# Kernel tuning notes

Measured on AMD Instinct MI355X. Metric: run time of the kernel, lower is better.

## Reference

```python
import jax, jax.numpy as jnp
import numpy as np

SEQ, BATCH, HID = 4096, 32, 512


def setup_inputs() -> dict:
    key = jax.random.key(0)
    ks = jax.random.split(key, 7)
    s = 1.0 / np.sqrt(HID)
    return {
        "x0": jax.random.normal(ks[0], (SEQ, BATCH, 1), dtype=jnp.float32),
        "W_ih": jax.random.uniform(ks[1], (4 * HID, 1), jnp.float32, -s, s),
        "W_hh": jax.random.uniform(ks[2], (4 * HID, HID), jnp.float32, -s, s),
        "b_ih": jax.random.uniform(ks[3], (4 * HID,), jnp.float32, -s, s),
        "b_hh": jax.random.uniform(ks[4], (4 * HID,), jnp.float32, -s, s),
        "W_lin": jax.random.uniform(ks[5], (1, HID), jnp.float32, -s, s),
        "b_lin": jax.random.uniform(ks[6], (1,), jnp.float32, -s, s),
    }


def _lstm(x0, W_ih, W_hh, b_ih, b_hh):
    # x0: (T, B, 1). Precompute input contribution to gates for all steps.
    x_proj = jnp.einsum("tbi,gi->tbg", x0, W_ih) + (b_ih + b_hh)  # (T, B, 4H)
    T, B, _ = x_proj.shape
    H = W_hh.shape[1]
    h0 = jnp.zeros((B, H), x0.dtype)
    c0 = jnp.zeros((B, H), x0.dtype)

    def step(carry, xp):
        h, c = carry
        gates = xp + h @ W_hh.T  # (B, 4H)
        i, f, g, o = jnp.split(gates, 4, axis=-1)  # torch gate order i,f,g,o
        i = jax.nn.sigmoid(i)
        f = jax.nn.sigmoid(f)
        g = jnp.tanh(g)
        o = jax.nn.sigmoid(o)
        c = f * c + i * g
        h = o * jnp.tanh(c)
        return (h, c), h

    _, hs = jax.lax.scan(step, (h0, c0), x_proj)  # hs: (T, B, H)
    return hs


def reference(x0, W_ih, W_hh, b_ih, b_hh, W_lin, b_lin):
    hs = _lstm(x0, W_ih, W_hh, b_ih, b_hh)            # (T, B, H)
    y = jnp.einsum("tbh,oh->tbo", hs, W_lin) + b_lin  # (T, B, 1)
    return y + x0                                      # residual add
```

## Files before the change

### kernel.cpp

```cpp
#include <hip/hip_runtime.h>
#include <stdint.h>

#define T_STEPS 4096
#define BATCH 32
#define HID 512
#define GROUPS 8
#define BLK_THREADS 1024
#define NBLOCKS 256
#define SLOT_DW (BATCH * GROUPS * 64)

typedef _Float16 h2_t __attribute__((ext_vector_type(2)));
typedef uint32_t u32x8 __attribute__((ext_vector_type(8)));

__device__ inline uint32_t pack_h2(float a, float b) {
  h2_t v;
  v.x = (_Float16)a;
  v.y = (_Float16)b;
  return __builtin_bit_cast(uint32_t, v);
}

__device__ inline float fdot2(uint32_t a, uint32_t b, float c) {
  return __builtin_amdgcn_fdot2(__builtin_bit_cast(h2_t, a),
                                __builtin_bit_cast(h2_t, b), c, false);
}

__device__ inline uint64_t uni64(const void* p) {
  uint32_t lo = __builtin_amdgcn_readfirstlane((uint32_t)(uintptr_t)p);
  uint32_t hi = __builtin_amdgcn_readfirstlane((uint32_t)((uintptr_t)p >> 32));
  return ((uint64_t)hi << 32) | lo;
}

__device__ inline void kinv() {
  asm volatile("s_dcache_inv" ::: "memory");
}

__device__ inline void sload_rec(uint64_t p, u32x8* d0, u32x8* d1,
                                 u32x8* d2, u32x8* d3,
                                 uint32_t* t0, uint32_t* t1,
                                 uint32_t* t2, uint32_t* t3) {
  asm volatile("s_load_dwordx8 %0, %8, 0x0\n\t"
               "s_load_dword %4, %8, 0x20\n\t"
               "s_load_dwordx8 %1, %8, 0x40\n\t"
               "s_load_dword %5, %8, 0x60\n\t"
               "s_load_dwordx8 %2, %8, 0x80\n\t"
               "s_load_dword %6, %8, 0xa0\n\t"
               "s_load_dwordx8 %3, %8, 0xc0\n\t"
               "s_load_dword %7, %8, 0xe0\n\t"
               "s_waitcnt lgkmcnt(0)"
               : "=&s"(*d0), "=&s"(*d1), "=&s"(*d2), "=&s"(*d3),
                 "=&s"(*t0), "=&s"(*t1), "=&s"(*t2), "=&s"(*t3)
               : "s"(p) : "memory");
}

__device__ inline float sigf(float x) { return 1.0f / (1.0f + __expf(-x)); }
__device__ inline float tanh_fast(float x) {
  float a = fabsf(x);
  float e = __expf(-2.0f * a);
  float r = (1.0f - e) / (1.0f + e);
  return copysignf(r, x);
}

__global__ __launch_bounds__(BLK_THREADS)
void lstm_nobar(const float* __restrict__ x0,
                const float* __restrict__ W_ih,
                const float* __restrict__ W_hh,
                const float* __restrict__ b_ih,
                const float* __restrict__ b_hh,
                const float* __restrict__ W_lin,
                const float* __restrict__ b_lin,
                float* __restrict__ y,
                uint32_t* __restrict__ h_ex,
                int* __restrict__ claim)
{
  __shared__ float x0_lds[T_STEPS];
  __shared__ float ylds[T_STEPS];
  __shared__ float gacc[2][256];
  __shared__ int arrive[2];
  __shared__ int s_bg;

  const int tid = threadIdx.x;

  if (tid == 0) {
    uint32_t xcc;
    asm volatile("s_getreg_b32 %0, hwreg(HW_REG_XCC_ID)" : "=s"(xcc));
    xcc &= 7;
    int slot = atomicAdd(claim + xcc * 16, 1);
    s_bg = (slot < 32) ? (int)(((4 * xcc + (slot >> 3)) << 3) | (slot & 7))
                       : -1;
  }
  __syncthreads();
  if (s_bg < 0) return;
  const int b  = s_bg >> 3;
  const int g  = s_bg & 7;
  const int u0 = g * 64;
  const int wv = tid >> 6;
  const int rg = wv >> 3;
  const int cs = wv & 7;
  const int l  = tid & 63;

  uint32_t w0[32], w1[32];
  {
    const int r0 = 128 * rg + l;
    const int r1 = r0 + 64;
    const int R0 = (r0 >> 6) * HID + u0 + (r0 & 63);
    const int R1 = (r1 >> 6) * HID + u0 + (r1 & 63);
    const float2* p0 = (const float2*)(W_hh + (size_t)R0 * HID + 64 * cs);
    const float2* p1 = (const float2*)(W_hh + (size_t)R1 * HID + 64 * cs);
#pragma unroll
    for (int k = 0; k < 32; ++k) {
      float2 a = p0[k], c = p1[k];
      w0[k] = pack_h2(a.x, a.y);
      w1[k] = pack_h2(c.x, c.y);
    }
  }
  for (int i = tid; i < T_STEPS; i += BLK_THREADS) {
    x0_lds[i] = x0[i * BATCH + b];
    ylds[i] = 0.f;
  }
  if (tid < 256) { gacc[0][tid] = 0.f; gacc[1][tid] = 0.f; }
  if (tid < 2) arrive[tid] = 0;

  float c_state = 0.f;
  float wih_[4] = {0.f, 0.f, 0.f, 0.f}, bs_[4] = {0.f, 0.f, 0.f, 0.f};
  float wlin_u = 0.f, blin = 0.f;
  if (tid < 64) {
#pragma unroll
    for (int j = 0; j < 4; ++j) {
      int R = j * HID + u0 + tid;
      wih_[j] = W_ih[R];
      bs_[j] = b_ih[R] + b_hh[R];
    }
    wlin_u = W_lin[u0 + tid];
    blin = b_lin[0];
  }

  uint32_t* hb = h_ex + (size_t)b * (GROUPS * 64);
  const uint64_t dpu[2] = { uni64(hb + 64 * cs),
                            uni64(hb + SLOT_DW + 64 * cs) };
  uint32_t* pub01[2] = { hb + 64 * g, hb + SLOT_DW + 64 * g };

  __syncthreads();

  int dead = 0;
  for (int t = 0; t < T_STEPS; ++t) {
    const int sl = t & 1, ns = sl ^ 1;

    u32x8 D0, D1, D2, D3;
    uint32_t tg0, tg1, tg2, tg3;
    {
      const uint32_t want = (uint32_t)t;
      int guard = 0;
      for (;;) {
        kinv();
        sload_rec(dpu[sl], &D0, &D1, &D2, &D3, &tg0, &tg1, &tg2, &tg3);
        if ((tg0 == want) & (tg1 == want) &
            (tg2 == want) & (tg3 == want)) break;
        if (dead || ++guard > (1 << 17)) { dead = 1; break; }
        __builtin_amdgcn_s_sleep(2);
      }
    }

    __builtin_amdgcn_s_setprio(1);
    float acc0a = 0.f, acc0b = 0.f, acc1a = 0.f, acc1b = 0.f;
#pragma unroll
    for (int k = 0; k < 8; ++k) {
      acc0a = fdot2(w0[k],      D0[k], acc0a);
      acc1a = fdot2(w1[k],      D0[k], acc1a);
      acc0b = fdot2(w0[8 + k],  D1[k], acc0b);
      acc1b = fdot2(w1[8 + k],  D1[k], acc1b);
      acc0a = fdot2(w0[16 + k], D2[k], acc0a);
      acc1a = fdot2(w1[16 + k], D2[k], acc1a);
      acc0b = fdot2(w0[24 + k], D3[k], acc0b);
      acc1b = fdot2(w1[24 + k], D3[k], acc1b);
    }
    atomicAdd(&gacc[sl][128 * rg + l], acc0a + acc0b);
    atomicAdd(&gacc[sl][128 * rg + 64 + l], acc1a + acc1b);
    asm volatile("" ::: "memory");
    if (l == 0) atomicAdd(&arrive[sl], 1);
    __builtin_amdgcn_s_setprio(0);

    if (tid < 64) {
      {
        int guard = 0;
        while (((volatile int*)arrive)[sl] < 16) {
          if (++guard > (1 << 20)) break;
        }
      }
      asm volatile("" ::: "memory");
      __builtin_amdgcn_s_setprio(1);
      arrive[sl] = 0;

      const float xv = x0_lds[t];
      float gi = gacc[sl][tid]       + xv * wih_[0] + bs_[0];
      float gf = gacc[sl][tid + 64]  + xv * wih_[1] + bs_[1];
      float gg = gacc[sl][tid + 128] + xv * wih_[2] + bs_[2];
      float go = gacc[sl][tid + 192] + xv * wih_[3] + bs_[3];
      float si = sigf(gi), sf = sigf(gf), tg_ = tanh_fast(gg), so = sigf(go);
      c_state = sf * c_state + si * tg_;
      float h = so * tanh_fast(c_state);

      float hn = __shfl_down(h, 1, 64);
      uint32_t val = 0;
      int doff = 0;
      bool act = false;
      if ((tid & 1) == 0) {
        int j = tid >> 1;
        val = pack_h2(h, hn);
        doff = ((j >> 3) << 4) + (j & 7);
        act = true;
      } else if (tid < 8) {
        int L = (tid - 1) >> 1;
        val = (uint32_t)(t + 1);
        doff = (L << 4) + 8;
        act = true;
      }
      if (act) pub01[ns][doff] = val;

      gacc[sl][tid] = 0.f;
      gacc[sl][tid + 64] = 0.f;
      gacc[sl][tid + 128] = 0.f;
      gacc[sl][tid + 192] = 0.f;

      float p = wlin_u * h;
#pragma unroll
      for (int m = 32; m >= 1; m >>= 1) p += __shfl_xor(p, m, 64);
      if (tid == 0) ylds[t] = p;
      __builtin_amdgcn_s_setprio(0);
    }
  }

  __syncthreads();
  for (int i = tid; i < T_STEPS; i += BLK_THREADS) {
    float val = ylds[i];
    if (g == 0) val += blin + x0_lds[i];
    unsafeAtomicAdd(&y[i * BATCH + b], val);
  }
}

extern "C" void kernel_launch(void* const* d_in, const int* in_sizes, int n_in,
                              void* d_out, int out_size, void* d_ws, size_t ws_size,
                              hipStream_t stream) {
  const float* x0    = (const float*)d_in[0];
  const float* W_ih  = (const float*)d_in[1];
  const float* W_hh  = (const float*)d_in[2];
  const float* b_ih  = (const float*)d_in[3];
  const float* b_hh  = (const float*)d_in[4];
  const float* W_lin = (const float*)d_in[5];
  const float* b_lin = (const float*)d_in[6];
  float* y = (float*)d_out;

  uint32_t* h_ex = (uint32_t*)d_ws;
  int* claim     = (int*)(h_ex + 2 * SLOT_DW);
  const size_t init_bytes = (size_t)2 * SLOT_DW * sizeof(uint32_t)
                            + 8 * 16 * sizeof(int);

  (void)hipMemsetAsync(d_ws, 0, init_bytes, stream);
  (void)hipMemsetAsync(d_out, 0, (size_t)out_size * sizeof(float), stream);

  hipLaunchKernelGGL(lstm_nobar, dim3(NBLOCKS), dim3(BLK_THREADS), 0, stream,
                     x0, W_ih, W_hh, b_ih, b_hh, W_lin, b_lin, y, h_ex, claim);
}
```

Before: 13.98 ms.

## Halve block to 8 waves, each computing all four gates for its column slice

Each block now runs 8 waves instead of 16. Every wave holds the weights for all four gates (128 packed registers) over one 64-column slice, so each scalar-loaded h chunk is reused four times and fewer waves contend on the LDS atomics and the arrival counter. The spin loop also drops its s_sleep and uses a shorter guard, so it polls more eagerly. The cost is higher register pressure per wave and fewer waves to hide latency. The shorter guard also makes it more likely that a slow step trips the dead-flag bailout.

After: 13.97 ms. No clear change (-0.1%).

```diff
diff --git a/kernel.cpp b/kernel.cpp
--- a/kernel.cpp
+++ b/kernel.cpp
@@ -5,7 +5,7 @@
 #define BATCH 32
 #define HID 512
 #define GROUPS 8
-#define BLK_THREADS 1024
+#define BLK_THREADS 512
 #define NBLOCKS 256
 #define SLOT_DW (BATCH * GROUPS * 64)
 
@@ -61,16 +61,16 @@
 }
 
 __global__ __launch_bounds__(BLK_THREADS)
-void lstm_nobar(const float* __restrict__ x0,
-                const float* __restrict__ W_ih,
-                const float* __restrict__ W_hh,
-                const float* __restrict__ b_ih,
-                const float* __restrict__ b_hh,
-                const float* __restrict__ W_lin,
-                const float* __restrict__ b_lin,
-                float* __restrict__ y,
-                uint32_t* __restrict__ h_ex,
-                int* __restrict__ claim)
+void lstm_w8(const float* __restrict__ x0,
+             const float* __restrict__ W_ih,
+             const float* __restrict__ W_hh,
+             const float* __restrict__ b_ih,
+             const float* __restrict__ b_hh,
+             const float* __restrict__ W_lin,
+             const float* __restrict__ b_lin,
+             float* __restrict__ y,
+             uint32_t* __restrict__ h_ex,
+             int* __restrict__ claim)
 {
   __shared__ float x0_lds[T_STEPS];
   __shared__ float ylds[T_STEPS];
@@ -94,23 +94,18 @@
   const int g  = s_bg & 7;
   const int u0 = g * 64;
   const int wv = tid >> 6;
-  const int rg = wv >> 3;
-  const int cs = wv & 7;
+  const int cs = wv;
   const int l  = tid & 63;
 
-  uint32_t w0[32], w1[32];
-  {
-    const int r0 = 128 * rg + l;
-    const int r1 = r0 + 64;
-    const int R0 = (r0 >> 6) * HID + u0 + (r0 & 63);
-    const int R1 = (r1 >> 6) * HID + u0 + (r1 & 63);
-    const float2* p0 = (const float2*)(W_hh + (size_t)R0 * HID + 64 * cs);
-    const float2* p1 = (const float2*)(W_hh + (size_t)R1 * HID + 64 * cs);
+  uint32_t w[4][32];
+#pragma unroll
+  for (int a = 0; a < 4; ++a) {
+    const int R = a * HID + u0 + l;
+    const float2* p = (const float2*)(W_hh + (size_t)R * HID + 64 * cs);
 #pragma unroll
     for (int k = 0; k < 32; ++k) {
-      float2 a = p0[k], c = p1[k];
-      w0[k] = pack_h2(a.x, a.y);
-      w1[k] = pack_h2(c.x, c.y);
+      float2 q = p[k];
+      w[a][k] = pack_h2(q.x, q.y);
     }
   }
   for (int i = tid; i < T_STEPS; i += BLK_THREADS) {
@@ -155,26 +150,36 @@
         sload_rec(dpu[sl], &D0, &D1, &D2, &D3, &tg0, &tg1, &tg2, &tg3);
         if ((tg0 == want) & (tg1 == want) &
             (tg2 == want) & (tg3 == want)) break;
-        if (dead || ++guard > (1 << 17)) { dead = 1; break; }
-        __builtin_amdgcn_s_sleep(2);
+        if (dead || ++guard > (1 << 14)) { dead = 1; break; }
       }
     }
 
     __builtin_amdgcn_s_setprio(1);
-    float acc0a = 0.f, acc0b = 0.f, acc1a = 0.f, acc1b = 0.f;
-#pragma unroll
-    for (int k = 0; k < 8; ++k) {
-      acc0a = fdot2(w0[k],      D0[k], acc0a);
-      acc1a = fdot2(w1[k],      D0[k], acc1a);
-      acc0b = fdot2(w0[8 + k],  D1[k], acc0b);
-      acc1b = fdot2(w1[8 + k],  D1[k], acc1b);
-      acc0a = fdot2(w0[16 + k], D2[k], acc0a);
-      acc1a = fdot2(w1[16 + k], D2[k], acc1a);
-      acc0b = fdot2(w0[24 + k], D3[k], acc0b);
-      acc1b = fdot2(w1[24 + k], D3[k], acc1b);
-    }
-    atomicAdd(&gacc[sl][128 * rg + l], acc0a + acc0b);
-    atomicAdd(&gacc[sl][128 * rg + 64 + l], acc1a + acc1b);
+    float ae0 = 0.f, ao0 = 0.f, ae1 = 0.f, ao1 = 0.f;
+    float ae2 = 0.f, ao2 = 0.f, ae3 = 0.f, ao3 = 0.f;
+#pragma unroll
+    for (int k = 0; k < 8; k += 2) {
+      ae0 = fdot2(w[0][k], D0[k], ae0);      ao0 = fdot2(w[0][k + 1], D0[k + 1], ao0);
+      ae1 = fdot2(w[1][k], D0[k], ae1);      ao1 = fdot2(w[1][k + 1], D0[k + 1], ao1);
+      ae2 = fdot2(w[2][k], D0[k], ae2);      ao2 = fdot2(w[2][k + 1], D0[k + 1], ao2);
+      ae3 = fdot2(w[3][k], D0[k], ae3);      ao3 = fdot2(w[3][k + 1], D0[k + 1], ao3);
+      ae0 = fdot2(w[0][8 + k], D1[k], ae0);  ao0 = fdot2(w[0][9 + k], D1[k + 1], ao0);
+      ae1 = fdot2(w[1][8 + k], D1[k], ae1);  ao1 = fdot2(w[1][9 + k], D1[k + 1], ao1);
+      ae2 = fdot2(w[2][8 + k], D1[k], ae2);  ao2 = fdot2(w[2][9 + k], D1[k + 1], ao2);
+      ae3 = fdot2(w[3][8 + k], D1[k], ae3);  ao3 = fdot2(w[3][9 + k], D1[k + 1], ao3);
+      ae0 = fdot2(w[0][16 + k], D2[k], ae0); ao0 = fdot2(w[0][17 + k], D2[k + 1], ao0);
+      ae1 = fdot2(w[1][16 + k], D2[k], ae1); ao1 = fdot2(w[1][17 + k], D2[k + 1], ao1);
+      ae2 = fdot2(w[2][16 + k], D2[k], ae2); ao2 = fdot2(w[2][17 + k], D2[k + 1], ao2);
+      ae3 = fdot2(w[3][16 + k], D2[k], ae3); ao3 = fdot2(w[3][17 + k], D2[k + 1], ao3);
+      ae0 = fdot2(w[0][24 + k], D3[k], ae0); ao0 = fdot2(w[0][25 + k], D3[k + 1], ao0);
+      ae1 = fdot2(w[1][24 + k], D3[k], ae1); ao1 = fdot2(w[1][25 + k], D3[k + 1], ao1);
+      ae2 = fdot2(w[2][24 + k], D3[k], ae2); ao2 = fdot2(w[2][25 + k], D3[k + 1], ao2);
+      ae3 = fdot2(w[3][24 + k], D3[k], ae3); ao3 = fdot2(w[3][25 + k], D3[k + 1], ao3);
+    }
+    atomicAdd(&gacc[sl][l],       ae0 + ao0);
+    atomicAdd(&gacc[sl][64 + l],  ae1 + ao1);
+    atomicAdd(&gacc[sl][128 + l], ae2 + ao2);
+    atomicAdd(&gacc[sl][192 + l], ae3 + ao3);
     asm volatile("" ::: "memory");
     if (l == 0) atomicAdd(&arrive[sl], 1);
     __builtin_amdgcn_s_setprio(0);
@@ -182,7 +187,7 @@
     if (tid < 64) {
       {
         int guard = 0;
-        while (((volatile int*)arrive)[sl] < 16) {
+        while (((volatile int*)arrive)[sl] < 8) {
           if (++guard > (1 << 20)) break;
         }
       }
@@ -257,6 +262,6 @@
   (void)hipMemsetAsync(d_ws, 0, init_bytes, stream);
   (void)hipMemsetAsync(d_out, 0, (size_t)out_size * sizeof(float), stream);
 
-  hipLaunchKernelGGL(lstm_nobar, dim3(NBLOCKS), dim3(BLK_THREADS), 0, stream,
+  hipLaunchKernelGGL(lstm_w8, dim3(NBLOCKS), dim3(BLK_THREADS), 0, stream,
                      x0, W_ih, W_hh, b_ih, b_hh, W_lin, b_lin, y, h_ex, claim);
 }
```
